# Kernel optimization log

Hardware: AMD Instinct MI355X
Metric: run time of the kernel (lower is better)

Reference implementation:

```python
import jax, jax.numpy as jnp
import numpy as np

N_NODES = 50000
N_EDGES = 800000
IN_DIM = 128
HID_DIM = 128
EMB_DIM = 64


def _glorot(key, shape):
    fan_in, fan_out = shape
    lim = np.sqrt(6.0 / (fan_in + fan_out))
    return jax.random.uniform(key, shape, jnp.float32, -lim, lim)


def setup_inputs() -> dict:
    key = jax.random.key(0)
    ks = jax.random.split(key, 5)
    x = jax.random.normal(ks[0], (N_NODES, IN_DIM), jnp.float32)
    edge_index = jax.random.randint(ks[1], (2, N_EDGES), 0, N_NODES, jnp.int64)
    W1 = _glorot(ks[2], (IN_DIM, HID_DIM))
    W2 = _glorot(ks[3], (HID_DIM, EMB_DIM))
    W3 = _glorot(ks[4], (EMB_DIM, IN_DIM))
    b1 = jnp.zeros((HID_DIM,), jnp.float32)
    b2 = jnp.zeros((EMB_DIM,), jnp.float32)
    b3 = jnp.zeros((IN_DIM,), jnp.float32)
    return {"x": x, "edge_index": edge_index,
            "W1": W1, "b1": b1, "W2": W2, "b2": b2, "W3": W3, "b3": b3}


def _gcn_conv(x, W, b, src, dst, norm, n_nodes):
    # PyG GCNConv: transform then normalized neighbor aggregation (with self-loops)
    h = x @ W                                   # [N, out]
    msg = h[src] * norm[:, None]                # gather + scale, [E+N, out]
    out = jax.ops.segment_sum(msg, dst, num_segments=n_nodes)  # scatter-add
    return out + b


def _gcn_norm(edge_index, n_nodes):
    # add self-loops, compute sym-normalized edge weights D^-1/2 (A+I) D^-1/2
    loop = jnp.arange(n_nodes, dtype=edge_index.dtype)
    src = jnp.concatenate([edge_index[0], loop])
    dst = jnp.concatenate([edge_index[1], loop])
    deg = jax.ops.segment_sum(jnp.ones_like(dst, jnp.float32), dst,
                              num_segments=n_nodes)
    dinv = jnp.where(deg > 0, jax.lax.rsqrt(jnp.maximum(deg, 1.0)), 0.0)
    norm = dinv[src] * dinv[dst]
    return src, dst, norm


def reference(x, edge_index, W1, b1, W2, b2, W3, b3):
    n_nodes = x.shape[0]
    src, dst, norm = _gcn_norm(edge_index, n_nodes)
    h = jax.nn.relu(_gcn_conv(x, W1, b1, src, dst, norm, n_nodes))
    h = jax.nn.relu(_gcn_conv(h, W2, b2, src, dst, norm, n_nodes))
    out = _gcn_conv(h, W3, b3, src, dst, norm, n_nodes)
    return out
```

## Files before the change

kernel.cpp:

```cpp
#include <hip/hip_runtime.h>
#include <hip/hip_bf16.h>

static inline int ceil_div(int a, int b) { return (a + b - 1) / b; }


#define SORT_BLOCKS 256

__global__ __launch_bounds__(256) void bucket_hist_kernel(const int* __restrict__ ei,
        int* __restrict__ hist_b, int E, int nbucket, int chunk) {
    __shared__ int h[256];
    const int t = (int)threadIdx.x;
    h[t] = 0;
    __syncthreads();
    const int b = blockIdx.x;
    const int e0 = b * chunk, e1 = min(E, e0 + chunk);
    for (int e = e0 + t; e < e1; e += 256)
        atomicAdd(&h[ei[E + e] >> 8], 1);
    __syncthreads();
    if (t < nbucket) hist_b[t * SORT_BLOCKS + b] = h[t];
}

__global__ __launch_bounds__(256) void row_scan_kernel(int* __restrict__ hist_b,
        int* __restrict__ btot) {
    const int i = blockIdx.x;
    const int t = (int)threadIdx.x;
    int c = hist_b[i * SORT_BLOCKS + t];
    int v = c;
    const int lane = t & 63, wid = t >> 6;
    #pragma unroll
    for (int off = 1; off < 64; off <<= 1) {
        int u = __shfl_up(v, off);
        if (lane >= off) v += u;
    }
    __shared__ int wsum[4];
    if (lane == 63) wsum[wid] = v;
    __syncthreads();
    int wbase = 0;
    #pragma unroll
    for (int w = 0; w < 4; ++w) if (w < wid) wbase += wsum[w];
    v += wbase;
    hist_b[i * SORT_BLOCKS + t] = v - c;
    if (t == 255) btot[i] = v;
}

__global__ __launch_bounds__(256) void bucket_scatter_kernel(const int* __restrict__ ei,
        const int* __restrict__ rel_base, const int* __restrict__ btot,
        int* __restrict__ bstart, unsigned int* __restrict__ tmp,
        int E, int nbucket, int chunk) {
    __shared__ int sc[256];
    __shared__ int cur[256];
    const int t = (int)threadIdx.x;
    const int b = blockIdx.x;
    int tot = (t < nbucket) ? btot[t] : 0;
    sc[t] = tot;
    __syncthreads();
    for (int off = 1; off < 256; off <<= 1) {
        int v = (t >= off) ? sc[t - off] : 0;
        __syncthreads();
        sc[t] += v;
        __syncthreads();
    }
    const int my_bstart = sc[t] - tot;
    if (b == 0) {
        if (t < nbucket) bstart[t] = my_bstart;
        if (t == 0) bstart[nbucket] = E;
    }
    if (t < nbucket) cur[t] = my_bstart + rel_base[t * SORT_BLOCKS + b];
    __syncthreads();
    const int e0 = b * chunk, e1 = min(E, e0 + chunk);
    for (int e = e0 + t; e < e1; e += 256) {
        int s = ei[e];
        int d = ei[E + e];
        int pos = atomicAdd(&cur[d >> 8], 1);
        tmp[pos] = (unsigned int)s | ((unsigned int)(d & 255) << 16);
    }
}

__global__ __launch_bounds__(256) void csr_build_kernel(const unsigned int* __restrict__ tmp,
        const int* __restrict__ bucket_start, int* __restrict__ rowptr,
        float* __restrict__ dinv, int* __restrict__ colidx, int n, int E) {
    __shared__ int hist[256], sc[256], cur[256];
    const int h = blockIdx.x;
    const int t = (int)threadIdx.x;
    hist[t] = 0;
    __syncthreads();
    const int e0 = bucket_start[h], e1 = bucket_start[h + 1];
    for (int e = e0 + t; e < e1; e += 256)
        atomicAdd(&hist[(tmp[e] >> 16) & 255], 1);
    __syncthreads();
    sc[t] = hist[t];
    __syncthreads();
    for (int off = 1; off < 256; off <<= 1) {
        int v = (t >= off) ? sc[t - off] : 0;
        __syncthreads();
        sc[t] += v;
        __syncthreads();
    }
    const int excl = sc[t] - hist[t];
    const int node = h * 256 + t;
    if (node < n) {
        rowptr[node] = e0 + excl;
        dinv[node] = rsqrtf((float)(hist[t] + 1));
    }
    if (h == 0 && t == 0) rowptr[n] = E;
    cur[t] = excl;
    __syncthreads();
    for (int e = e0 + t; e < e1; e += 256) {
        unsigned int p = tmp[e];
        int pos = e0 + atomicAdd(&cur[(p >> 16) & 255], 1);
        colidx[pos] = (int)(p & 0xFFFFu);
    }
}


template<int K, int N, bool BIAS, bool OUT_BF16>
__global__ __launch_bounds__(256) void gemm_kernel(const float* __restrict__ A,
        const float* __restrict__ W, const float* __restrict__ bias,
        void* __restrict__ out_, int M) {
    __shared__ float As[16][68];
    __shared__ float Bs[16][68];
    const int bm = blockIdx.x * 64;
    const int bn = blockIdx.y * 64;
    const int tid = (int)threadIdx.x;
    const int tx = tid & 15;
    const int ty = tid >> 4;
    float acc[4][4] = {};
    for (int k0 = 0; k0 < K; k0 += 16) {
        {
            int m   = tid >> 2;
            int kk4 = (tid & 3) * 4;
            float4 v = make_float4(0.f, 0.f, 0.f, 0.f);
            if (bm + m < M)
                v = *(const float4*)&A[(size_t)(bm + m) * K + k0 + kk4];
            As[kk4 + 0][m] = v.x;
            As[kk4 + 1][m] = v.y;
            As[kk4 + 2][m] = v.z;
            As[kk4 + 3][m] = v.w;
        }
        {
            int kk = tid >> 4;
            int n4 = (tid & 15) * 4;
            *(float4*)&Bs[kk][n4] = *(const float4*)&W[(size_t)(k0 + kk) * N + bn + n4];
        }
        __syncthreads();
        #pragma unroll
        for (int kk = 0; kk < 16; ++kk) {
            float4 a4 = *(const float4*)&As[kk][ty * 4];
            float4 b4 = *(const float4*)&Bs[kk][tx * 4];
            float a[4] = {a4.x, a4.y, a4.z, a4.w};
            float b[4] = {b4.x, b4.y, b4.z, b4.w};
            #pragma unroll
            for (int i = 0; i < 4; ++i)
                #pragma unroll
                for (int j = 0; j < 4; ++j)
                    acc[i][j] += a[i] * b[j];
        }
        __syncthreads();
    }
    #pragma unroll
    for (int i = 0; i < 4; ++i) {
        int m = bm + ty * 4 + i;
        if (m >= M) continue;
        float v[4];
        #pragma unroll
        for (int j = 0; j < 4; ++j) {
            v[j] = acc[i][j];
            if (BIAS) v[j] += bias[bn + tx * 4 + j];
        }
        size_t base = (size_t)m * N + bn + tx * 4;
        if constexpr (OUT_BF16) {
            __hip_bfloat16* ob = (__hip_bfloat16*)out_;
            __hip_bfloat162 p0, p1;
            p0.x = __float2bfloat16(v[0]); p0.y = __float2bfloat16(v[1]);
            p1.x = __float2bfloat16(v[2]); p1.y = __float2bfloat16(v[3]);
            *(__hip_bfloat162*)&ob[base]     = p0;
            *(__hip_bfloat162*)&ob[base + 2] = p1;
        } else {
            float* of = (float*)out_;
            *(float2*)&of[base]     = make_float2(v[0], v[1]);
            *(float2*)&of[base + 2] = make_float2(v[2], v[3]);
        }
    }
}


template<int D, bool BIAS, bool RELU, bool OUT_BF16>
__global__ __launch_bounds__(256) void agg_kernel(const void* __restrict__ in_,
        const float* __restrict__ bias,
        const int* __restrict__ rowptr, const int* __restrict__ colidx,
        const float* __restrict__ dinv, void* __restrict__ out_, int n) {
    constexpr int VPL = D / 64;
    const int lane = (int)threadIdx.x & 63;
    const int wid  = (int)threadIdx.x >> 6;
    const int i = blockIdx.x * 4 + wid;
    if (i >= n) return;
    const float di = dinv[i];
    float acc0 = 0.f, acc1 = 0.f;
    if constexpr (VPL == 2) {
        const __hip_bfloat162* in = (const __hip_bfloat162*)in_;
        __hip_bfloat162 sv = in[(size_t)i * 64 + lane];
        acc0 = di * __bfloat162float(sv.x);
        acc1 = di * __bfloat162float(sv.y);
    } else {
        const __hip_bfloat16* in = (const __hip_bfloat16*)in_;
        acc0 = di * __bfloat162float(in[(size_t)i * 64 + lane]);
    }
    int e = rowptr[i];
    const int e1 = rowptr[i + 1];
    for (; e + 8 <= e1; e += 8) {
        int s[8]; float w[8];
        #pragma unroll
        for (int j = 0; j < 8; ++j) s[j] = __builtin_amdgcn_readfirstlane(colidx[e + j]);
        #pragma unroll
        for (int j = 0; j < 8; ++j) w[j] = dinv[s[j]];
        if constexpr (VPL == 2) {
            const __hip_bfloat162* in = (const __hip_bfloat162*)in_;
            __hip_bfloat162 v[8];
            #pragma unroll
            for (int j = 0; j < 8; ++j) v[j] = in[(size_t)s[j] * 64 + lane];
            #pragma unroll
            for (int j = 0; j < 8; ++j) {
                acc0 += w[j] * __bfloat162float(v[j].x);
                acc1 += w[j] * __bfloat162float(v[j].y);
            }
        } else {
            const __hip_bfloat16* in = (const __hip_bfloat16*)in_;
            __hip_bfloat16 v[8];
            #pragma unroll
            for (int j = 0; j < 8; ++j) v[j] = in[(size_t)s[j] * 64 + lane];
            #pragma unroll
            for (int j = 0; j < 8; ++j) acc0 += w[j] * __bfloat162float(v[j]);
        }
    }
    for (; e < e1; ++e) {
        int s = __builtin_amdgcn_readfirstlane(colidx[e]);
        float w = dinv[s];
        if constexpr (VPL == 2) {
            const __hip_bfloat162* in = (const __hip_bfloat162*)in_;
            __hip_bfloat162 v = in[(size_t)s * 64 + lane];
            acc0 += w * __bfloat162float(v.x);
            acc1 += w * __bfloat162float(v.y);
        } else {
            const __hip_bfloat16* in = (const __hip_bfloat16*)in_;
            acc0 += w * __bfloat162float(in[(size_t)s * 64 + lane]);
        }
    }
    float v0 = di * acc0;
    float v1 = di * acc1;
    if constexpr (VPL == 2) {
        if (BIAS) { v0 += bias[2 * lane]; v1 += bias[2 * lane + 1]; }
        if (RELU) { v0 = fmaxf(v0, 0.f); v1 = fmaxf(v1, 0.f); }
        if constexpr (OUT_BF16) {
            __hip_bfloat162* ob = (__hip_bfloat162*)out_;
            __hip_bfloat162 p; p.x = __float2bfloat16(v0); p.y = __float2bfloat16(v1);
            ob[(size_t)i * 64 + lane] = p;
        } else {
            float2* of = (float2*)out_;
            of[(size_t)i * 64 + lane] = make_float2(v0, v1);
        }
    } else {
        if (BIAS) v0 += bias[lane];
        if (RELU) v0 = fmaxf(v0, 0.f);
        if constexpr (OUT_BF16) {
            __hip_bfloat16* ob = (__hip_bfloat16*)out_;
            ob[(size_t)i * 64 + lane] = __float2bfloat16(v0);
        } else {
            float* of = (float*)out_;
            of[(size_t)i * 64 + lane] = v0;
        }
    }
}


extern "C" void kernel_launch(void* const* d_in, const int* in_sizes, int n_in,
                              void* d_out, int out_size, void* d_ws, size_t ws_size,
                              hipStream_t stream) {
    const float* x  = (const float*)d_in[0];
    const int*   ei = (const int*)d_in[1];
    const float* W1 = (const float*)d_in[2];
    const float* b1 = (const float*)d_in[3];
    const float* W2 = (const float*)d_in[4];
    const float* b2 = (const float*)d_in[5];
    const float* W3 = (const float*)d_in[6];
    const float* b3 = (const float*)d_in[7];

    const int IN = 128;
    const int n  = in_sizes[0] / IN;
    const int E  = in_sizes[1] / 2;

    char* ws = (char*)d_ws;
    size_t off = 0;
    auto alloc = [&](size_t bytes) {
        char* p = ws + off;
        off += (bytes + 255) & ~(size_t)255;
        return p;
    };
    __hip_bfloat16* hA_bf = (__hip_bfloat16*)alloc((size_t)n * 128 * 2);
    float*          bufB  = (float*)alloc((size_t)n * 128 * 4);
    __hip_bfloat16* hC_bf = (__hip_bfloat16*)alloc((size_t)n * 64 * 2);
    __hip_bfloat16* hD_bf = (__hip_bfloat16*)alloc((size_t)n * 64 * 2);
    float*          bufE  = (float*)alloc((size_t)n * 64 * 4);
    int*   rowptr = (int*)  alloc(((size_t)n + 1) * sizeof(int));
    float* dinv   = (float*)alloc((size_t)n * sizeof(float));
    int*   colidx = (int*)  alloc((size_t)E * sizeof(int));
    unsigned int* tmp = (unsigned int*)alloc((size_t)E * sizeof(unsigned int));
    int*   hist_b = (int*)  alloc((size_t)256 * SORT_BLOCKS * sizeof(int));
    int*   btot   = (int*)  alloc(256 * sizeof(int));
    int*   bstart = (int*)  alloc(257 * sizeof(int));

    const int nbucket = ceil_div(n, 256);
    const int chunk   = ceil_div(E, SORT_BLOCKS);

    bucket_hist_kernel<<<SORT_BLOCKS, 256, 0, stream>>>(ei, hist_b, E, nbucket, chunk);
    row_scan_kernel<<<nbucket, 256, 0, stream>>>(hist_b, btot);
    bucket_scatter_kernel<<<SORT_BLOCKS, 256, 0, stream>>>(ei, hist_b, btot, bstart, tmp, E, nbucket, chunk);
    csr_build_kernel<<<nbucket, 256, 0, stream>>>(tmp, bstart, rowptr, dinv, colidx, n, E);

    dim3 g1(ceil_div(n, 64), 2);
    gemm_kernel<128, 128, false, true><<<g1, 256, 0, stream>>>(x, W1, nullptr, hA_bf, n);
    agg_kernel<128, true, true, false><<<ceil_div(n, 4), 256, 0, stream>>>(
        hA_bf, b1, rowptr, colidx, dinv, bufB, n);

    dim3 g2(ceil_div(n, 64), 1);
    gemm_kernel<128, 64, false, true><<<g2, 256, 0, stream>>>(bufB, W2, nullptr, hC_bf, n);
    agg_kernel<64, true, true, true><<<ceil_div(n, 4), 256, 0, stream>>>(
        hC_bf, b2, rowptr, colidx, dinv, hD_bf, n);

    agg_kernel<64, false, false, false><<<ceil_div(n, 4), 256, 0, stream>>>(
        hD_bf, nullptr, rowptr, colidx, dinv, bufE, n);
    dim3 g3(ceil_div(n, 64), 2);
    gemm_kernel<64, 128, true, false><<<g3, 256, 0, stream>>>(bufE, W3, b3, d_out, n);
}
```

Before: 276.6 us.

## Replace FP32 SIMT GEMMs with split-bf16 MFMA matrix-core kernels

The three dense transforms are moved from scalar FP32 FMA tiles onto bf16 MFMA instructions. Each FP32 operand is split into high and low bf16 parts, and three MFMAs per fragment (hi*hi, lo*hi, hi*lo) keep accuracy close to FP32. Shared-memory tiles use an XOR swizzle to avoid bank conflicts. In exchange the kernel spends extra conversion work and uses 16x16 fragments with scalar per-element stores in the epilogue, which makes output writes less coalesced.

```diff
diff --git a/kernel.cpp b/kernel.cpp
--- a/kernel.cpp
+++ b/kernel.cpp
@@ -2,6 +2,19 @@
 #include <hip/hip_bf16.h>
 
 static inline int ceil_div(int a, int b) { return (a + b - 1) / b; }
+
+typedef __attribute__((ext_vector_type(8))) short short8v;
+typedef __attribute__((ext_vector_type(4))) float f32x4;
+
+__device__ inline short f2bf(float v) {
+    unsigned u = __builtin_bit_cast(unsigned, v);
+    unsigned r = (u + 0x7FFFu + ((u >> 16) & 1u)) >> 16;
+    return (short)r;
+}
+__device__ inline float bf2f(short s) {
+    unsigned u = ((unsigned)(unsigned short)s) << 16;
+    return __builtin_bit_cast(float, u);
+}
 
 
 #define SORT_BLOCKS 256
@@ -113,72 +126,114 @@
 }
 
 
+__device__ inline int swz(int r, int k) {
+    int byte = r * 64 + k * 2;
+    byte ^= (r & 7) << 4;
+    return byte >> 1;
+}
+
 template<int K, int N, bool BIAS, bool OUT_BF16>
-__global__ __launch_bounds__(256) void gemm_kernel(const float* __restrict__ A,
+__global__ __launch_bounds__(256) void gemm_mfma_kernel(const float* __restrict__ A,
         const float* __restrict__ W, const float* __restrict__ bias,
         void* __restrict__ out_, int M) {
-    __shared__ float As[16][68];
-    __shared__ float Bs[16][68];
+    __shared__ short Ah_s[2048], Al_s[2048], Bh_s[2048], Bl_s[2048];
+    const int tid  = (int)threadIdx.x;
+    const int lane = tid & 63;
+    const int wid  = tid >> 6;
     const int bm = blockIdx.x * 64;
     const int bn = blockIdx.y * 64;
-    const int tid = (int)threadIdx.x;
-    const int tx = tid & 15;
-    const int ty = tid >> 4;
-    float acc[4][4] = {};
-    for (int k0 = 0; k0 < K; k0 += 16) {
+    const int wr = (wid >> 1) * 32;
+    const int wc = (wid & 1) * 32;
+
+    f32x4 acc00 = {0.f,0.f,0.f,0.f}, acc01 = {0.f,0.f,0.f,0.f};
+    f32x4 acc10 = {0.f,0.f,0.f,0.f}, acc11 = {0.f,0.f,0.f,0.f};
+
+    const int a_row = tid >> 2;
+    const int a_k0  = (tid & 3) * 8;
+    const int b_k   = tid >> 3;
+    const int b_c0  = (tid & 7) * 8;
+
+    for (int kc = 0; kc < K; kc += 32) {
         {
-            int m   = tid >> 2;
-            int kk4 = (tid & 3) * 4;
-            float4 v = make_float4(0.f, 0.f, 0.f, 0.f);
-            if (bm + m < M)
-                v = *(const float4*)&A[(size_t)(bm + m) * K + k0 + kk4];
-            As[kk4 + 0][m] = v.x;
-            As[kk4 + 1][m] = v.y;
-            As[kk4 + 2][m] = v.z;
-            As[kk4 + 3][m] = v.w;
+            float v[8] = {0.f,0.f,0.f,0.f,0.f,0.f,0.f,0.f};
+            int grow = bm + a_row;
+            if (grow < M) {
+                float4 p0 = *(const float4*)&A[(size_t)grow * K + kc + a_k0];
+                float4 p1 = *(const float4*)&A[(size_t)grow * K + kc + a_k0 + 4];
+                v[0]=p0.x; v[1]=p0.y; v[2]=p0.z; v[3]=p0.w;
+                v[4]=p1.x; v[5]=p1.y; v[6]=p1.z; v[7]=p1.w;
+            }
+            short8v hv, lv;
+            #pragma unroll
+            for (int j = 0; j < 8; ++j) {
+                short h = f2bf(v[j]);
+                hv[j] = h;
+                lv[j] = f2bf(v[j] - bf2f(h));
+            }
+            *(short8v*)&Ah_s[swz(a_row, a_k0)] = hv;
+            *(short8v*)&Al_s[swz(a_row, a_k0)] = lv;
         }
         {
-            int kk = tid >> 4;
-            int n4 = (tid & 15) * 4;
-            *(float4*)&Bs[kk][n4] = *(const float4*)&W[(size_t)(k0 + kk) * N + bn + n4];
-        }
-        __syncthreads();
+            float4 p0 = *(const float4*)&W[(size_t)(kc + b_k) * N + bn + b_c0];
+            float4 p1 = *(const float4*)&W[(size_t)(kc + b_k) * N + bn + b_c0 + 4];
+            float v[8] = {p0.x,p0.y,p0.z,p0.w,p1.x,p1.y,p1.z,p1.w};
+            #pragma unroll
+            for (int j = 0; j < 8; ++j) {
+                short h = f2bf(v[j]);
+                Bh_s[swz(b_c0 + j, b_k)] = h;
+                Bl_s[swz(b_c0 + j, b_k)] = f2bf(v[j] - bf2f(h));
+            }
+        }
+        __syncthreads();
+        {
+            const int fr = lane & 15;
+            const int kb = (lane >> 4) * 8;
+            short8v ah0 = *(const short8v*)&Ah_s[swz(wr +  0 + fr, kb)];
+            short8v ah1 = *(const short8v*)&Ah_s[swz(wr + 16 + fr, kb)];
+            short8v al0 = *(const short8v*)&Al_s[swz(wr +  0 + fr, kb)];
+            short8v al1 = *(const short8v*)&Al_s[swz(wr + 16 + fr, kb)];
+            short8v bh0 = *(const short8v*)&Bh_s[swz(wc +  0 + fr, kb)];
+            short8v bh1 = *(const short8v*)&Bh_s[swz(wc + 16 + fr, kb)];
+            short8v bl0 = *(const short8v*)&Bl_s[swz(wc +  0 + fr, kb)];
+            short8v bl1 = *(const short8v*)&Bl_s[swz(wc + 16 + fr, kb)];
+            acc00 = __builtin_amdgcn_mfma_f32_16x16x32_bf16(ah0, bh0, acc00, 0, 0, 0);
+            acc00 = __builtin_amdgcn_mfma_f32_16x16x32_bf16(al0, bh0, acc00, 0, 0, 0);
+            acc00 = __builtin_amdgcn_mfma_f32_16x16x32_bf16(ah0, bl0, acc00, 0, 0, 0);
+            acc01 = __builtin_amdgcn_mfma_f32_16x16x32_bf16(ah0, bh1, acc01, 0, 0, 0);
+            acc01 = __builtin_amdgcn_mfma_f32_16x16x32_bf16(al0, bh1, acc01, 0, 0, 0);
+            acc01 = __builtin_amdgcn_mfma_f32_16x16x32_bf16(ah0, bl1, acc01, 0, 0, 0);
+            acc10 = __builtin_amdgcn_mfma_f32_16x16x32_bf16(ah1, bh0, acc10, 0, 0, 0);
+            acc10 = __builtin_amdgcn_mfma_f32_16x16x32_bf16(al1, bh0, acc10, 0, 0, 0);
+            acc10 = __builtin_amdgcn_mfma_f32_16x16x32_bf16(ah1, bl0, acc10, 0, 0, 0);
+            acc11 = __builtin_amdgcn_mfma_f32_16x16x32_bf16(ah1, bh1, acc11, 0, 0, 0);
+            acc11 = __builtin_amdgcn_mfma_f32_16x16x32_bf16(al1, bh1, acc11, 0, 0, 0);
+            acc11 = __builtin_amdgcn_mfma_f32_16x16x32_bf16(ah1, bl1, acc11, 0, 0, 0);
+        }
+        __syncthreads();
+    }
+
+    const int c0 = lane & 15;
+    const int r0 = (lane >> 4) * 4;
+    #pragma unroll
+    for (int fi = 0; fi < 2; ++fi) {
         #pragma unroll
-        for (int kk = 0; kk < 16; ++kk) {
-            float4 a4 = *(const float4*)&As[kk][ty * 4];
-            float4 b4 = *(const float4*)&Bs[kk][tx * 4];
-            float a[4] = {a4.x, a4.y, a4.z, a4.w};
-            float b[4] = {b4.x, b4.y, b4.z, b4.w};
-            #pragma unroll
-            for (int i = 0; i < 4; ++i)
-                #pragma unroll
-                for (int j = 0; j < 4; ++j)
-                    acc[i][j] += a[i] * b[j];
-        }
-        __syncthreads();
-    }
-    #pragma unroll
-    for (int i = 0; i < 4; ++i) {
-        int m = bm + ty * 4 + i;
-        if (m >= M) continue;
-        float v[4];
-        #pragma unroll
-        for (int j = 0; j < 4; ++j) {
-            v[j] = acc[i][j];
-            if (BIAS) v[j] += bias[bn + tx * 4 + j];
-        }
-        size_t base = (size_t)m * N + bn + tx * 4;
-        if constexpr (OUT_BF16) {
-            __hip_bfloat16* ob = (__hip_bfloat16*)out_;
-            __hip_bfloat162 p0, p1;
-            p0.x = __float2bfloat16(v[0]); p0.y = __float2bfloat16(v[1]);
-            p1.x = __float2bfloat16(v[2]); p1.y = __float2bfloat16(v[3]);
-            *(__hip_bfloat162*)&ob[base]     = p0;
-            *(__hip_bfloat162*)&ob[base + 2] = p1;
-        } else {
-            float* of = (float*)out_;
-            *(float2*)&of[base]     = make_float2(v[0], v[1]);
-            *(float2*)&of[base + 2] = make_float2(v[2], v[3]);
+        for (int fj = 0; fj < 2; ++fj) {
+            f32x4 a = (fi == 0) ? ((fj == 0) ? acc00 : acc01)
+                                : ((fj == 0) ? acc10 : acc11);
+            #pragma unroll
+            for (int r = 0; r < 4; ++r) {
+                int grow = bm + wr + fi * 16 + r0 + r;
+                int gcol = bn + wc + fj * 16 + c0;
+                if (grow < M) {
+                    float val = a[r];
+                    if (BIAS) val += bias[gcol];
+                    if constexpr (OUT_BF16) {
+                        ((__hip_bfloat16*)out_)[(size_t)grow * N + gcol] = __float2bfloat16(val);
+                    } else {
+                        ((float*)out_)[(size_t)grow * N + gcol] = val;
+                    }
+                }
+            }
         }
     }
 }
@@ -317,17 +372,17 @@
     csr_build_kernel<<<nbucket, 256, 0, stream>>>(tmp, bstart, rowptr, dinv, colidx, n, E);
 
     dim3 g1(ceil_div(n, 64), 2);
-    gemm_kernel<128, 128, false, true><<<g1, 256, 0, stream>>>(x, W1, nullptr, hA_bf, n);
+    gemm_mfma_kernel<128, 128, false, true><<<g1, 256, 0, stream>>>(x, W1, nullptr, hA_bf, n);
     agg_kernel<128, true, true, false><<<ceil_div(n, 4), 256, 0, stream>>>(
         hA_bf, b1, rowptr, colidx, dinv, bufB, n);
 
     dim3 g2(ceil_div(n, 64), 1);
-    gemm_kernel<128, 64, false, true><<<g2, 256, 0, stream>>>(bufB, W2, nullptr, hC_bf, n);
+    gemm_mfma_kernel<128, 64, false, true><<<g2, 256, 0, stream>>>(bufB, W2, nullptr, hC_bf, n);
     agg_kernel<64, true, true, true><<<ceil_div(n, 4), 256, 0, stream>>>(
         hC_bf, b2, rowptr, colidx, dinv, hD_bf, n);
 
     agg_kernel<64, false, false, false><<<ceil_div(n, 4), 256, 0, stream>>>(
         hD_bf, nullptr, rowptr, colidx, dinv, bufE, n);
     dim3 g3(ceil_div(n, 64), 2);
-    gemm_kernel<64, 128, true, false><<<g3, 256, 0, stream>>>(bufE, W3, b3, d_out, n);
-}
+    gemm_mfma_kernel<64, 128, true, false><<<g3, 256, 0, stream>>>(bufE, W3, b3, d_out, n);
+}
```

Result: faster. 270.7 us (-2.1%).
